# Kernel optimization log

Hardware: AMD Instinct MI355X
Metric: run time of the kernel (lower is better)

The kernel has to match this reference:

```python
import jax, jax.numpy as jnp
import numpy as np

B, S, IN, H, E, OUT = 64, 2048, 256, 512, 256, 32000


def setup_inputs() -> dict:
    key = jax.random.key(0)
    ks = jax.random.split(key, 20)
    g = lambda k, shp, fan_in: jax.random.normal(k, shp, jnp.float32) / jnp.sqrt(jnp.float32(fan_in))
    return {
        "x": jax.random.normal(ks[0], (B, IN), jnp.float32),
        "hidden": jax.random.normal(ks[1], (B, H), jnp.float32),
        "encoder_outputs": jax.random.normal(ks[2], (B, S, H), jnp.float32),
        # attention params
        "W1_w": g(ks[3], (H, E), H), "W1_b": jnp.zeros((E,), jnp.float32),
        "W2_w": g(ks[4], (H, E), H),
        "v_w": g(ks[5], (E, 1), E),
        # GRU gate params (input to gates is concat(x, context): IN+H)
        "Wxr_w": g(ks[6], (IN + H, H), IN + H), "Wxr_b": jnp.zeros((H,), jnp.float32),
        "Whr_w": g(ks[7], (H, H), H),
        "Wxz_w": g(ks[8], (IN + H, H), IN + H), "Wxz_b": jnp.zeros((H,), jnp.float32),
        "Whz_w": g(ks[9], (H, H), H),
        "Wxh_w": g(ks[10], (IN + H, H), IN + H), "Wxh_b": jnp.zeros((H,), jnp.float32),
        "Whh_w": g(ks[11], (H, H), H),
        # output projection
        "Who_w": g(ks[12], (H, OUT), H), "Who_b": jnp.zeros((OUT,), jnp.float32),
    }


def reference(x, hidden, encoder_outputs,
              W1_w, W1_b, W2_w, v_w,
              Wxr_w, Wxr_b, Whr_w,
              Wxz_w, Wxz_b, Whz_w,
              Wxh_w, Wxh_b, Whh_w,
              Who_w, Who_b):
    # Bahdanau attention
    # energy: [B, S, E]
    energy = jnp.tanh(jnp.einsum("bsh,he->bse", encoder_outputs, W1_w) + W1_b
                      + (hidden @ W2_w)[:, None, :])
    scores = jnp.einsum("bse,eo->bs", energy, v_w)          # [B, S]
    attn_weights = jax.nn.softmax(scores, axis=1)            # [B, S]
    context = jnp.einsum("bs,bsh->bh", attn_weights, encoder_outputs)  # [B, H]

    x_context = jnp.concatenate([x, context], axis=-1)       # [B, IN+H]
    reset_gate = jax.nn.sigmoid(x_context @ Wxr_w + Wxr_b + hidden @ Whr_w)
    update_gate = jax.nn.sigmoid(x_context @ Wxz_w + Wxz_b + hidden @ Whz_w)
    h_tilde = jnp.tanh(x_context @ Wxh_w + Wxh_b + (reset_gate * hidden) @ Whh_w)
    new_hidden = update_gate * hidden + (1.0 - update_gate) * h_tilde
    output = new_hidden @ Who_w + Who_b                      # [B, OUT]
    return (output, new_hidden, attn_weights)
```

## Files before the change

### kernel.cpp

```cpp
#include <hip/hip_runtime.h>

#define BB 64
#define SS 2048
#define INDIM 256
#define HH 512
#define EE 256
#define OUTD 32000

typedef __attribute__((ext_vector_type(8))) short short8;
typedef __attribute__((ext_vector_type(4))) float floatx4;

#define LOG2E 1.4426950408889634f

__device__ __forceinline__ unsigned short f2bf(float f) {
  unsigned u = __float_as_uint(f);
  return (unsigned short)((u + 0x7FFFu + ((u >> 16) & 1u)) >> 16);
}
__device__ __forceinline__ unsigned pk2(float a, float b) {
  return (unsigned)f2bf(a) | ((unsigned)f2bf(b) << 16);
}
__device__ __forceinline__ float bf2f(unsigned short u) {
  return __uint_as_float((unsigned)u << 16);
}
__device__ __forceinline__ float fast_tanh(float x) {
  float e = __builtin_amdgcn_exp2f(x * 2.8853900817779268f);
  return 1.0f - 2.0f * __builtin_amdgcn_rcpf(e + 1.0f);
}
__device__ __forceinline__ float fast_sigmoid(float x) {
  float e = __builtin_amdgcn_exp2f(-x * LOG2E);
  return __builtin_amdgcn_rcpf(1.0f + e);
}

#define WS_W1T   0
#define WS_HBP   262144
#define WS_CTX   393216
#define WS_NHBF  524288
#define WS_Z     589824
#define WS_RH    720896
#define WS_GP    851968
#define WS_NP    3473408
#define WS_CTXP  4784128
#define WS_SUMP  8978432

__global__ void k_prep(const float* __restrict__ W1, unsigned short* __restrict__ W1t) {
  int idx = blockIdx.x * 256 + threadIdx.x;
  int k = idx >> 8, e = idx & 255;
  W1t[e * HH + k] = f2bf(W1[idx]);
}

__global__ __launch_bounds__(256) void k_hb(const float* __restrict__ hidden,
                                            const float* __restrict__ W2,
                                            const float* __restrict__ W1b,
                                            float* __restrict__ hbp) {
  int b0 = blockIdx.x * 4, seg = blockIdx.y, e = threadIdx.x;
  int h0 = seg * 256;
  float a0 = 0, a1 = 0, a2 = 0, a3 = 0;
  if (seg == 0) { a0 = a1 = a2 = a3 = W1b[e]; }
  for (int h = 0; h < 256; ++h) {
    float w = W2[(h0 + h) * EE + e];
    a0 += hidden[(b0 + 0) * HH + h0 + h] * w;
    a1 += hidden[(b0 + 1) * HH + h0 + h] * w;
    a2 += hidden[(b0 + 2) * HH + h0 + h] * w;
    a3 += hidden[(b0 + 3) * HH + h0 + h] * w;
  }
  float* o = hbp + (size_t)seg * BB * EE;
  o[(b0 + 0) * EE + e] = a0; o[(b0 + 1) * EE + e] = a1;
  o[(b0 + 2) * EE + e] = a2; o[(b0 + 3) * EE + e] = a3;
}

#define LDA 520
__global__ __launch_bounds__(256) void k_scores(
    const float* __restrict__ enc, const unsigned short* __restrict__ W1t,
    const float* __restrict__ hbp, const float* __restrict__ vw,
    float* __restrict__ attn, float* __restrict__ ctxp, float* __restrict__ sump) {
  __shared__ unsigned short Afull[64 * LDA];
  __shared__ float hb_s[EE], v_s[EE];
  __shared__ float red[4 * 64];
  __shared__ float wbuf[64];

  int tid = threadIdx.x;
  int m0 = blockIdx.x * 64;
  int b = blockIdx.x >> 5;
  int sloc = (blockIdx.x & 31) * 64;
  hb_s[tid] = hbp[b * EE + tid] + hbp[BB * EE + b * EE + tid];
  v_s[tid] = vw[tid];

  int lane = tid & 63, wn = tid >> 6;
  int l15 = lane & 15, quad = lane >> 4;

  int row0 = tid >> 3, kg = tid & 7;
  const float* base0 = enc + (size_t)(m0 + row0) * HH + kg * 4;
  const float* base1 = enc + (size_t)(m0 + 32 + row0) * HH + kg * 4;

  floatx4 acc[4][4];
#pragma unroll
  for (int i = 0; i < 4; ++i)
#pragma unroll
    for (int j = 0; j < 4; ++j) acc[i][j] = (floatx4)0.0f;

  float4 pf0[3], pf1[3];
#pragma unroll
  for (int d = 0; d < 3; ++d) {
    pf0[d] = *(const float4*)(base0 + d * 32);
    pf1[d] = *(const float4*)(base1 + d * 32);
  }

#pragma unroll
  for (int kb = 0; kb < 16; ++kb) {
    int slot = kb % 3;
    {
      float4 f = pf0[slot];
      uint2 w; w.x = pk2(f.x, f.y); w.y = pk2(f.z, f.w);
      *(uint2*)(Afull + row0 * LDA + kb * 32 + kg * 4) = w;
      f = pf1[slot];
      uint2 w2; w2.x = pk2(f.x, f.y); w2.y = pk2(f.z, f.w);
      *(uint2*)(Afull + (row0 + 32) * LDA + kb * 32 + kg * 4) = w2;
    }
    if (kb + 3 < 16) {
      pf0[slot] = *(const float4*)(base0 + (kb + 3) * 32);
      pf1[slot] = *(const float4*)(base1 + (kb + 3) * 32);
    }
    __syncthreads();
    int kk = kb * 32 + quad * 8;
    short8 a[4];
#pragma unroll
    for (int i = 0; i < 4; ++i)
      a[i] = *(const short8*)(Afull + (i * 16 + l15) * LDA + kk);
#pragma unroll
    for (int j = 0; j < 4; ++j) {
      short8 bfr = *(const short8*)(W1t + (wn * 64 + j * 16 + l15) * HH + kk);
#pragma unroll
      for (int i = 0; i < 4; ++i)
        acc[i][j] = __builtin_amdgcn_mfma_f32_16x16x32_bf16(a[i], bfr, acc[i][j], 0, 0, 0);
    }
  }
  __syncthreads();

#pragma unroll
  for (int i = 0; i < 4; ++i)
#pragma unroll
    for (int r = 0; r < 4; ++r) {
      float s = 0.0f;
#pragma unroll
      for (int j = 0; j < 4; ++j) {
        int e = wn * 64 + j * 16 + l15;
        s += fast_tanh(acc[i][j][r] + hb_s[e]) * v_s[e];
      }
#pragma unroll
      for (int off = 1; off < 16; off <<= 1) s += __shfl_xor(s, off, 64);
      if (l15 == 0) red[wn * 64 + i * 16 + quad * 4 + r] = s;
    }
  __syncthreads();
  if (tid < 64) {
    float sc = red[tid] + red[64 + tid] + red[128 + tid] + red[192 + tid];
    float e = __builtin_amdgcn_exp2f(sc * LOG2E);
    wbuf[tid] = e;
    attn[b * SS + sloc + tid] = e;
    float s = e;
#pragma unroll
    for (int off = 1; off < 64; off <<= 1) s += __shfl_xor(s, off, 64);
    if (tid == 0) sump[blockIdx.x] = s;
  }
  __syncthreads();

  float cx0 = 0.0f, cx1 = 0.0f;
#pragma unroll 8
  for (int r = 0; r < 64; ++r) {
    float w = wbuf[r];
    cx0 += w * bf2f(Afull[r * LDA + tid]);
    cx1 += w * bf2f(Afull[r * LDA + 256 + tid]);
  }
  ctxp[(size_t)blockIdx.x * HH + tid] = cx0;
  ctxp[(size_t)blockIdx.x * HH + 256 + tid] = cx1;
}

__global__ __launch_bounds__(512) void k_norm(float* __restrict__ attn,
                                              const float* __restrict__ ctxp,
                                              const float* __restrict__ sump,
                                              float* __restrict__ ctx) {
  int b = blockIdx.x, tid = threadIdx.x;
  float s = 0.0f;
#pragma unroll
  for (int t = 0; t < 32; ++t) s += sump[b * 32 + t];
  float inv = 1.0f / s;
#pragma unroll
  for (int i = 0; i < 4; ++i) attn[b * SS + tid + i * 512] *= inv;
  float c = 0.0f;
#pragma unroll
  for (int t = 0; t < 32; ++t) c += ctxp[(size_t)(b * 32 + t) * HH + tid];
  ctx[b * HH + tid] = c * inv;
}

__device__ __forceinline__ void part_seg(
    const float* __restrict__ Wx, const float* __restrict__ Wh,
    const float* __restrict__ x, const float* __restrict__ ctx,
    const float* __restrict__ hv, int seg, int b0, int h,
    float* __restrict__ outp) {
  const float* wseg;
  const float* a0; const float* a1; const float* a2; const float* a3;
  int vk0 = seg * 128;
  if (seg < 2) {
    wseg = Wx + (size_t)vk0 * HH;
    a0 = x + (b0 + 0) * INDIM + vk0;       a1 = x + (b0 + 1) * INDIM + vk0;
    a2 = x + (b0 + 2) * INDIM + vk0;       a3 = x + (b0 + 3) * INDIM + vk0;
  } else if (seg < 6) {
    wseg = Wx + (size_t)vk0 * HH;
    int off = vk0 - 256;
    a0 = ctx + (b0 + 0) * HH + off;        a1 = ctx + (b0 + 1) * HH + off;
    a2 = ctx + (b0 + 2) * HH + off;        a3 = ctx + (b0 + 3) * HH + off;
  } else {
    int off = vk0 - 768;
    wseg = Wh + (size_t)off * HH;
    a0 = hv + (b0 + 0) * HH + off;         a1 = hv + (b0 + 1) * HH + off;
    a2 = hv + (b0 + 2) * HH + off;         a3 = hv + (b0 + 3) * HH + off;
  }
  float s0 = 0, s1 = 0, s2 = 0, s3 = 0;
  for (int i = 0; i < 128; ++i) {
    float w = wseg[i * HH + h];
    s0 += a0[i] * w; s1 += a1[i] * w;
    s2 += a2[i] * w; s3 += a3[i] * w;
  }
  outp[(b0 + 0) * HH + h] = s0; outp[(b0 + 1) * HH + h] = s1;
  outp[(b0 + 2) * HH + h] = s2; outp[(b0 + 3) * HH + h] = s3;
}

__global__ __launch_bounds__(512) void k_gpart(
    const float* __restrict__ x, const float* __restrict__ ctx,
    const float* __restrict__ hidden,
    const float* __restrict__ Wxr, const float* __restrict__ Whr,
    const float* __restrict__ Wxz, const float* __restrict__ Whz,
    float* __restrict__ gp) {
  int b0 = blockIdx.x * 4, seg = blockIdx.y, sel = blockIdx.z, h = threadIdx.x;
  const float* Wx = sel ? Wxz : Wxr;
  const float* Wh = sel ? Whz : Whr;
  float* outp = gp + (size_t)(sel * 10 + seg) * BB * HH;
  part_seg(Wx, Wh, x, ctx, hidden, seg, b0, h, outp);
}

__global__ __launch_bounds__(512) void k_gred(
    const float* __restrict__ gp, const float* __restrict__ Wxrb,
    const float* __restrict__ Wxzb, const float* __restrict__ hidden,
    float* __restrict__ z_out, float* __restrict__ rh_out) {
  int b = blockIdx.x, h = threadIdx.x;
  float r = Wxrb[h], z = Wxzb[h];
#pragma unroll
  for (int s = 0; s < 10; ++s) {
    r += gp[((size_t)s * BB + b) * HH + h];
    z += gp[((size_t)(10 + s) * BB + b) * HH + h];
  }
  r = fast_sigmoid(r);
  z_out[b * HH + h] = fast_sigmoid(z);
  rh_out[b * HH + h] = r * hidden[b * HH + h];
}

__global__ __launch_bounds__(512) void k_npart(
    const float* __restrict__ x, const float* __restrict__ ctx,
    const float* __restrict__ rh,
    const float* __restrict__ Wxh, const float* __restrict__ Whh,
    float* __restrict__ np) {
  int b0 = blockIdx.x * 4, seg = blockIdx.y, h = threadIdx.x;
  float* outp = np + (size_t)seg * BB * HH;
  part_seg(Wxh, Whh, x, ctx, rh, seg, b0, h, outp);
}

__global__ __launch_bounds__(512) void k_nred(
    const float* __restrict__ np, const float* __restrict__ Wxhb,
    const float* __restrict__ z, const float* __restrict__ hidden,
    float* __restrict__ nh, unsigned short* __restrict__ nhbf) {
  int b = blockIdx.x, h = threadIdx.x;
  float a = Wxhb[h];
#pragma unroll
  for (int s = 0; s < 10; ++s) a += np[((size_t)s * BB + b) * HH + h];
  float ht = fast_tanh(a);
  float zz = z[b * HH + h];
  float val = zz * hidden[b * HH + h] + (1.0f - zz) * ht;
  nh[b * HH + h] = val;
  nhbf[b * HH + h] = f2bf(val);
}

__global__ __launch_bounds__(256) void k_out2(const unsigned short* __restrict__ nhbf,
                                              const float* __restrict__ Who,
                                              const float* __restrict__ Whob,
                                              float* __restrict__ out) {
  int tid = threadIdx.x;
  int lane = tid & 63, w = tid >> 6;
  int l15 = lane & 15, quad = lane >> 4;
  int n = blockIdx.x * 64 + w * 16 + l15;

  floatx4 acc[4];
#pragma unroll
  for (int i = 0; i < 4; ++i) acc[i] = (floatx4)0.0f;

#pragma unroll
  for (int kc = 0; kc < 16; ++kc) {
    int k0 = kc * 32;
    float bf[8];
    const float* bp = Who + (size_t)(k0 + quad * 8) * OUTD + n;
#pragma unroll
    for (int j = 0; j < 8; ++j) bf[j] = bp[(size_t)j * OUTD];
    union { unsigned u[4]; short8 v; } bu;
#pragma unroll
    for (int j = 0; j < 4; ++j) bu.u[j] = pk2(bf[2 * j], bf[2 * j + 1]);
#pragma unroll
    for (int i = 0; i < 4; ++i) {
      short8 af = *(const short8*)(nhbf + (i * 16 + l15) * HH + k0 + quad * 8);
      acc[i] = __builtin_amdgcn_mfma_f32_16x16x32_bf16(af, bu.v, acc[i], 0, 0, 0);
    }
  }
  float bias = Whob[n];
#pragma unroll
  for (int i = 0; i < 4; ++i)
#pragma unroll
    for (int r = 0; r < 4; ++r) {
      int m = i * 16 + quad * 4 + r;
      out[(size_t)m * OUTD + n] = acc[i][r] + bias;
    }
}

extern "C" void kernel_launch(void* const* d_in, const int* in_sizes, int n_in,
                              void* d_out, int out_size, void* d_ws, size_t ws_size,
                              hipStream_t stream) {
  const float* x    = (const float*)d_in[0];
  const float* hid  = (const float*)d_in[1];
  const float* enc  = (const float*)d_in[2];
  const float* W1w  = (const float*)d_in[3];
  const float* W1b  = (const float*)d_in[4];
  const float* W2w  = (const float*)d_in[5];
  const float* vw   = (const float*)d_in[6];
  const float* Wxr  = (const float*)d_in[7];
  const float* Wxrb = (const float*)d_in[8];
  const float* Whr  = (const float*)d_in[9];
  const float* Wxz  = (const float*)d_in[10];
  const float* Wxzb = (const float*)d_in[11];
  const float* Whz  = (const float*)d_in[12];
  const float* Wxh  = (const float*)d_in[13];
  const float* Wxhb = (const float*)d_in[14];
  const float* Whh  = (const float*)d_in[15];
  const float* Who  = (const float*)d_in[16];
  const float* Whob = (const float*)d_in[17];

  float* out  = (float*)d_out;
  float* nh   = out + (size_t)BB * OUTD;
  float* attn = nh + (size_t)BB * HH;

  char* ws = (char*)d_ws;
  unsigned short* W1t  = (unsigned short*)(ws + WS_W1T);
  float* hbp  = (float*)(ws + WS_HBP);
  float* ctx  = (float*)(ws + WS_CTX);
  unsigned short* nhbf = (unsigned short*)(ws + WS_NHBF);
  float* zg   = (float*)(ws + WS_Z);
  float* rh   = (float*)(ws + WS_RH);
  float* gp   = (float*)(ws + WS_GP);
  float* np   = (float*)(ws + WS_NP);
  float* ctxp = (float*)(ws + WS_CTXP);
  float* sump = (float*)(ws + WS_SUMP);

  k_prep<<<512, 256, 0, stream>>>(W1w, W1t);
  k_hb<<<dim3(16, 2), 256, 0, stream>>>(hid, W2w, W1b, hbp);
  k_scores<<<(BB * SS) / 64, 256, 0, stream>>>(enc, W1t, hbp, vw, attn, ctxp, sump);
  k_norm<<<BB, 512, 0, stream>>>(attn, ctxp, sump, ctx);
  k_gpart<<<dim3(16, 10, 2), 512, 0, stream>>>(x, ctx, hid, Wxr, Whr, Wxz, Whz, gp);
  k_gred<<<BB, 512, 0, stream>>>(gp, Wxrb, Wxzb, hid, zg, rh);
  k_npart<<<dim3(16, 10), 512, 0, stream>>>(x, ctx, rh, Wxh, Whh, np);
  k_nred<<<BB, 512, 0, stream>>>(np, Wxhb, zg, hid, nh, nhbf);
  k_out2<<<500, 256, 0, stream>>>(nhbf, Who, Whob, out);
}
```

Baseline: 550.5 us.

## Load encoder tiles directly into MFMA registers and split context partials per wave

The scores kernel drops the shared-memory staging of encoder rows and the per-k-block __syncthreads. Each wave now loads and converts its A fragments straight from global memory, so all four waves read the same encoder rows redundantly (possibly served by cache). Each wave writes one quarter of the tile to shared memory for the context pass, which now uses vectorized short8 reads over 16 rows per wave. This produces four times as many context partials, which the norm kernel sums over 128 entries. The change also adds a two-blocks-per-CU occupancy hint and relocates the sum workspace.

Measured after the change: 683.4 us. 1.24x slower.

```diff
diff --git a/kernel.cpp b/kernel.cpp
--- a/kernel.cpp
+++ b/kernel.cpp
@@ -40,7 +40,7 @@
 #define WS_GP    851968
 #define WS_NP    3473408
 #define WS_CTXP  4784128
-#define WS_SUMP  8978432
+#define WS_SUMP  21561344
 
 __global__ void k_prep(const float* __restrict__ W1, unsigned short* __restrict__ W1t) {
   int idx = blockIdx.x * 256 + threadIdx.x;
@@ -68,12 +68,11 @@
   o[(b0 + 2) * EE + e] = a2; o[(b0 + 3) * EE + e] = a3;
 }
 
-#define LDA 520
-__global__ __launch_bounds__(256) void k_scores(
+__global__ __launch_bounds__(256, 2) void k_scores(
     const float* __restrict__ enc, const unsigned short* __restrict__ W1t,
     const float* __restrict__ hbp, const float* __restrict__ vw,
     float* __restrict__ attn, float* __restrict__ ctxp, float* __restrict__ sump) {
-  __shared__ unsigned short Afull[64 * LDA];
+  __shared__ unsigned short Afull[64 * 512];
   __shared__ float hb_s[EE], v_s[EE];
   __shared__ float red[4 * 64];
   __shared__ float wbuf[64];
@@ -88,47 +87,42 @@
   int lane = tid & 63, wn = tid >> 6;
   int l15 = lane & 15, quad = lane >> 4;
 
-  int row0 = tid >> 3, kg = tid & 7;
-  const float* base0 = enc + (size_t)(m0 + row0) * HH + kg * 4;
-  const float* base1 = enc + (size_t)(m0 + 32 + row0) * HH + kg * 4;
-
   floatx4 acc[4][4];
 #pragma unroll
   for (int i = 0; i < 4; ++i)
 #pragma unroll
     for (int j = 0; j < 4; ++j) acc[i][j] = (floatx4)0.0f;
 
-  float4 pf0[3], pf1[3];
-#pragma unroll
-  for (int d = 0; d < 3; ++d) {
-    pf0[d] = *(const float4*)(base0 + d * 32);
-    pf1[d] = *(const float4*)(base1 + d * 32);
-  }
+  const float* arow0 = enc + (size_t)(m0 + 0 * 16 + l15) * HH + quad * 8;
+  const float* arow1 = enc + (size_t)(m0 + 1 * 16 + l15) * HH + quad * 8;
+  const float* arow2 = enc + (size_t)(m0 + 2 * 16 + l15) * HH + quad * 8;
+  const float* arow3 = enc + (size_t)(m0 + 3 * 16 + l15) * HH + quad * 8;
+  const unsigned short* brow0 = W1t + (size_t)(wn * 64 + 0 * 16 + l15) * HH + quad * 8;
+  const unsigned short* brow1 = W1t + (size_t)(wn * 64 + 1 * 16 + l15) * HH + quad * 8;
+  const unsigned short* brow2 = W1t + (size_t)(wn * 64 + 2 * 16 + l15) * HH + quad * 8;
+  const unsigned short* brow3 = W1t + (size_t)(wn * 64 + 3 * 16 + l15) * HH + quad * 8;
 
 #pragma unroll
   for (int kb = 0; kb < 16; ++kb) {
-    int slot = kb % 3;
-    {
-      float4 f = pf0[slot];
-      uint2 w; w.x = pk2(f.x, f.y); w.y = pk2(f.z, f.w);
-      *(uint2*)(Afull + row0 * LDA + kb * 32 + kg * 4) = w;
-      f = pf1[slot];
-      uint2 w2; w2.x = pk2(f.x, f.y); w2.y = pk2(f.z, f.w);
-      *(uint2*)(Afull + (row0 + 32) * LDA + kb * 32 + kg * 4) = w2;
-    }
-    if (kb + 3 < 16) {
-      pf0[slot] = *(const float4*)(base0 + (kb + 3) * 32);
-      pf1[slot] = *(const float4*)(base1 + (kb + 3) * 32);
-    }
-    __syncthreads();
-    int kk = kb * 32 + quad * 8;
+    int kk = kb * 32;
     short8 a[4];
 #pragma unroll
-    for (int i = 0; i < 4; ++i)
-      a[i] = *(const short8*)(Afull + (i * 16 + l15) * LDA + kk);
+    for (int i = 0; i < 4; ++i) {
+      const float* ap = (i == 0) ? arow0 : (i == 1) ? arow1 : (i == 2) ? arow2 : arow3;
+      float4 f0 = *(const float4*)(ap + kk);
+      float4 f1 = *(const float4*)(ap + kk + 4);
+      union { unsigned u[4]; short8 v; } au;
+      au.u[0] = pk2(f0.x, f0.y); au.u[1] = pk2(f0.z, f0.w);
+      au.u[2] = pk2(f1.x, f1.y); au.u[3] = pk2(f1.z, f1.w);
+      a[i] = au.v;
+      if (wn == i) {
+        *(short8*)(Afull + (wn * 16 + l15) * 512 + kk + quad * 8) = a[i];
+      }
+    }
 #pragma unroll
     for (int j = 0; j < 4; ++j) {
-      short8 bfr = *(const short8*)(W1t + (wn * 64 + j * 16 + l15) * HH + kk);
+      const unsigned short* bp = (j == 0) ? brow0 : (j == 1) ? brow1 : (j == 2) ? brow2 : brow3;
+      short8 bfr = *(const short8*)(bp + kk);
 #pragma unroll
       for (int i = 0; i < 4; ++i)
         acc[i][j] = __builtin_amdgcn_mfma_f32_16x16x32_bf16(a[i], bfr, acc[i][j], 0, 0, 0);
@@ -163,15 +157,23 @@
   }
   __syncthreads();
 
-  float cx0 = 0.0f, cx1 = 0.0f;
-#pragma unroll 8
-  for (int r = 0; r < 64; ++r) {
+  float cacc[8];
+#pragma unroll
+  for (int j = 0; j < 8; ++j) cacc[j] = 0.0f;
+#pragma unroll
+  for (int rr = 0; rr < 16; ++rr) {
+    int r = wn * 16 + rr;
     float w = wbuf[r];
-    cx0 += w * bf2f(Afull[r * LDA + tid]);
-    cx1 += w * bf2f(Afull[r * LDA + 256 + tid]);
-  }
-  ctxp[(size_t)blockIdx.x * HH + tid] = cx0;
-  ctxp[(size_t)blockIdx.x * HH + 256 + tid] = cx1;
+    short8 av = *(const short8*)(Afull + r * 512 + lane * 8);
+#pragma unroll
+    for (int j = 0; j < 8; ++j) cacc[j] += w * bf2f((unsigned short)av[j]);
+  }
+  float4 c0, c1;
+  c0.x = cacc[0]; c0.y = cacc[1]; c0.z = cacc[2]; c0.w = cacc[3];
+  c1.x = cacc[4]; c1.y = cacc[5]; c1.z = cacc[6]; c1.w = cacc[7];
+  float* cp = ctxp + ((size_t)blockIdx.x * 4 + wn) * HH + lane * 8;
+  *(float4*)cp = c0;
+  *(float4*)(cp + 4) = c1;
 }
 
 __global__ __launch_bounds__(512) void k_norm(float* __restrict__ attn,
@@ -186,8 +188,8 @@
 #pragma unroll
   for (int i = 0; i < 4; ++i) attn[b * SS + tid + i * 512] *= inv;
   float c = 0.0f;
-#pragma unroll
-  for (int t = 0; t < 32; ++t) c += ctxp[(size_t)(b * 32 + t) * HH + tid];
+#pragma unroll 8
+  for (int t = 0; t < 128; ++t) c += ctxp[(size_t)(b * 128 + t) * HH + tid];
   ctx[b * HH + tid] = c * inv;
 }
 
```
